# Performance work log

Measured on AMD Instinct MI355X. Metric: run time of the kernel, lower is better.

The kernel has to match this reference:

```python
import jax, jax.numpy as jnp
import numpy as np
from jax import lax

D_MODEL = 1024
D_STATE = 16
D_CONV = 4
EXPAND = 2
D_INNER = EXPAND * D_MODEL
LN_EPS = 1e-5


def setup_inputs() -> dict:
    key = jax.random.key(0)
    ks = jax.random.split(key, 12)
    B, L = 4, 1024
    s = lambda fan_in: 1.0 / np.sqrt(fan_in)
    inp = {
        "x": jax.random.normal(ks[0], (B, L, D_MODEL), jnp.float32),
        # in_proj: d_model -> 2*d_inner (stored as (in, out))
        "W_in": jax.random.normal(ks[1], (D_MODEL, 2 * D_INNER), jnp.float32) * s(D_MODEL),
        "b_in": jnp.zeros((2 * D_INNER,), jnp.float32),
        # depthwise causal conv1d, kernel (d_inner, 1, d_conv)
        "conv_w": jax.random.normal(ks[2], (D_INNER, 1, D_CONV), jnp.float32) * s(D_CONV),
        "conv_b": jnp.zeros((D_INNER,), jnp.float32),
        # x_proj: d_inner -> 2*d_state
        "W_xp": jax.random.normal(ks[3], (D_INNER, 2 * D_STATE), jnp.float32) * s(D_INNER),
        "b_xp": jnp.zeros((2 * D_STATE,), jnp.float32),
        # dt_proj: d_inner -> d_inner
        "W_dt": jax.random.normal(ks[4], (D_INNER, D_INNER), jnp.float32) * s(D_INNER),
        "b_dt": jnp.zeros((D_INNER,), jnp.float32),
        # A_log = log(arange(1, d_state+1)) repeated over d_inner
        "A_log": jnp.log(jnp.broadcast_to(jnp.arange(1, D_STATE + 1, dtype=jnp.float32), (D_INNER, D_STATE))),
        "D_param": jnp.ones((D_INNER,), jnp.float32),
        # out_proj: d_inner -> d_model
        "W_out": jax.random.normal(ks[5], (D_INNER, D_MODEL), jnp.float32) * s(D_INNER),
        "b_out": jnp.zeros((D_MODEL,), jnp.float32),
        "ln_g": jnp.ones((D_MODEL,), jnp.float32),
        "ln_b": jnp.zeros((D_MODEL,), jnp.float32),
    }
    return inp


def _causal_depthwise_conv(x, w, b):
    # x: (B, d_inner, L); w: (d_inner, 1, d_conv). Left-pad d_conv-1 => causal.
    y = lax.conv_general_dilated(
        x, w, window_strides=(1,), padding=[(D_CONV - 1, 0)],
        dimension_numbers=("NCH", "OIH", "NCH"), feature_group_count=D_INNER)
    return y + b[None, :, None]


def _ssm(x, A, Bm, Cm, dt, D_param):
    # x, dt: (B,L,D)  A: (D,N)  Bm, Cm: (B,L,N)
    A_disc = jnp.exp(dt[..., None] * A)               # (B,L,D,N)
    dBx = (dt * x)[..., None] * Bm[:, :, None, :]     # (B,L,D,N) = dt*B*x_t
    h0 = jnp.zeros(x.shape[:1] + A.shape, x.dtype)    # (B,D,N)

    def step(h, inputs):
        a, bx, c = inputs                              # (B,D,N),(B,D,N),(B,N)
        h = a * h + bx
        y = jnp.einsum("bdn,bn->bd", h, c)
        return h, y

    _, ys = lax.scan(step, h0, (jnp.swapaxes(A_disc, 0, 1),
                                jnp.swapaxes(dBx, 0, 1),
                                jnp.swapaxes(Cm, 0, 1)))
    y = jnp.swapaxes(ys, 0, 1)                         # (B,L,D)
    return y + x * D_param


def reference(x, W_in, b_in, conv_w, conv_b, W_xp, b_xp, W_dt, b_dt,
              A_log, D_param, W_out, b_out, ln_g, ln_b):
    residual = x
    xr = x @ W_in + b_in                               # (B,L,2*d_inner)
    xi, res = jnp.split(xr, 2, axis=-1)
    xi = jax.nn.silu(xi)
    xi = jnp.swapaxes(xi, 1, 2)                        # (B,d_inner,L)
    xi = _causal_depthwise_conv(xi, conv_w, conv_b)
    xi = jnp.swapaxes(xi, 1, 2)
    xi = jax.nn.silu(xi)
    bc = xi @ W_xp + b_xp                              # (B,L,2*d_state)
    Bm, Cm = jnp.split(bc, 2, axis=-1)
    dt = jax.nn.softplus(xi @ W_dt + b_dt)
    A = -jnp.exp(A_log)                                # (d_inner, d_state)
    y = _ssm(xi, A, Bm, Cm, dt, D_param)
    y = y * jax.nn.silu(res)
    out = y @ W_out + b_out
    z = out + residual
    mu = jnp.mean(z, axis=-1, keepdims=True)
    var = jnp.var(z, axis=-1, keepdims=True)
    return (z - mu) * jax.lax.rsqrt(var + LN_EPS) * ln_g + ln_b
```

## Files before the change

### kernel.cpp

```cpp
#include <hip/hip_runtime.h>
#include <math.h>

#define D_MODEL 1024
#define D_INNER 2048
#define D_STATE 16
#define D_CONV  4
#define NCHUNK  16
#define LCHUNK  64

typedef unsigned short u16;
typedef __attribute__((ext_vector_type(8))) short short8;
typedef __attribute__((ext_vector_type(4))) float f32x4;
typedef __attribute__((ext_vector_type(4))) unsigned short u16x4;

__device__ __forceinline__ float silu_f(float x) { return x / (1.f + __expf(-x)); }
__device__ __forceinline__ float softplus_f(float x) {
    return fmaxf(x, 0.f) + log1pf(__expf(-fabsf(x)));
}
__device__ __forceinline__ u16 f2bf(float f) {
    union { float f; unsigned u; } c; c.f = f;
    unsigned r = c.u + 0x7fffu + ((c.u >> 16) & 1u);
    return (u16)(r >> 16);
}
__device__ __forceinline__ float bf2f(u16 v) {
    union { unsigned u; float f; } c; c.u = ((unsigned)v) << 16; return c.f;
}
__device__ __forceinline__ void gload_lds16(const void* g, void* l) {
    __builtin_amdgcn_global_load_lds((const __attribute__((address_space(1))) void*)g,
                                     (__attribute__((address_space(3))) void*)l, 16, 0, 0);
}

__global__ __launch_bounds__(256)
void f32_to_bf16_kernel(const float* __restrict__ in, u16* __restrict__ out, int n4)
{
    const int i = blockIdx.x * 256 + threadIdx.x;
    if (i >= n4) return;
    const float4 v = *(const float4*)&in[(size_t)i * 4];
    u16x4 o; o.x = f2bf(v.x); o.y = f2bf(v.y); o.z = f2bf(v.z); o.w = f2bf(v.w);
    *(u16x4*)&out[(size_t)i * 4] = o;
}

__global__ __launch_bounds__(256)
void transpose_bf16_kernel(const float* __restrict__ W, u16* __restrict__ Wt, int K, int N)
{
    __shared__ float tile[32][33];
    const int tx = threadIdx.x & 31, ty = threadIdx.x >> 5;
    const int n0 = blockIdx.x * 32, k0 = blockIdx.y * 32;
#pragma unroll
    for (int q = 0; q < 4; q++)
        tile[ty + q * 8][tx] = W[(size_t)(k0 + ty + q * 8) * N + n0 + tx];
    __syncthreads();
#pragma unroll
    for (int q = 0; q < 4; q++)
        Wt[(size_t)(n0 + ty + q * 8) * K + k0 + tx] = f2bf(tile[tx][ty + q * 8]);
}

template <int MODE>
__global__ __launch_bounds__(512, 2)
void gemm_mfma256(const u16* __restrict__ A, const u16* __restrict__ Bt,
                  const float* __restrict__ bias,
                  void* __restrict__ out0v, void* __restrict__ out1v,
                  int M, int N, int K)
{
    __shared__ __align__(16) short As[2][256 * 64];
    __shared__ __align__(16) short Bs[2][256 * 64];

    const int tid = threadIdx.x;
    const int wid = tid >> 6, lane = tid & 63;
    const int wr = wid >> 2, wc = wid & 3;
    const int row0 = blockIdx.y * 256, col0 = blockIdx.x * 256;
    const int kg = lane >> 4, r16 = lane & 15;

    f32x4 acc[8][4] = {};

    const u16* Abase = A + (size_t)row0 * K;
    const u16* Bbase = Bt + (size_t)col0 * K;

#define STAGE256(bi, kk) do {                                                   \
        _Pragma("unroll")                                                       \
        for (int q = 0; q < 4; q++) {                                           \
            const int c = (q << 9) + tid;                                       \
            const int r = c >> 3;                                               \
            const int ks8 = (((c & 7) ^ (r & 7)) << 3);                         \
            gload_lds16(Abase + (size_t)r * K + (kk) + ks8,                     \
                        &As[bi][(((q << 9) + (wid << 6))) << 3]);               \
            gload_lds16(Bbase + (size_t)r * K + (kk) + ks8,                     \
                        &Bs[bi][(((q << 9) + (wid << 6))) << 3]);               \
        }                                                                       \
    } while (0)

    const int nt = K >> 6;
    STAGE256(0, 0);
    asm volatile("s_waitcnt vmcnt(0)" ::: "memory");
    __builtin_amdgcn_s_barrier();

    int cur = 0;
    for (int t = 0; t < nt; ++t) {
        if (t + 1 < nt) STAGE256(cur ^ 1, (t + 1) << 6);

        const int rx = r16 & 7;
#pragma unroll
        for (int ks = 0; ks < 2; ks++) {
            const int sl8 = (((ks << 2) + kg) ^ rx) << 3;
            short8 af[8], bg[4];
#pragma unroll
            for (int i = 0; i < 8; i++) {
                const int r = wr * 128 + i * 16 + r16;
                af[i] = *(const short8*)&As[cur][r * 64 + sl8];
            }
#pragma unroll
            for (int j = 0; j < 4; j++) {
                const int r = wc * 64 + j * 16 + r16;
                bg[j] = *(const short8*)&Bs[cur][r * 64 + sl8];
            }
            __builtin_amdgcn_s_setprio(1);
#pragma unroll
            for (int i = 0; i < 8; i++)
#pragma unroll
                for (int j = 0; j < 4; j++)
                    acc[i][j] = __builtin_amdgcn_mfma_f32_16x16x32_bf16(af[i], bg[j], acc[i][j], 0, 0, 0);
            __builtin_amdgcn_s_setprio(0);
        }

        asm volatile("s_waitcnt vmcnt(0)" ::: "memory");
        __builtin_amdgcn_s_barrier();
        cur ^= 1;
    }
#undef STAGE256

#pragma unroll
    for (int i = 0; i < 8; i++) {
#pragma unroll
        for (int j = 0; j < 4; j++) {
#pragma unroll
            for (int r = 0; r < 4; r++) {
                const int row = row0 + wr * 128 + i * 16 + kg * 4 + r;
                const int col = col0 + wc * 64 + j * 16 + r16;
                float v = acc[i][j][r] + bias[col];
                if (MODE == 0) {
                    u16* o0 = (u16*)out0v; u16* o1 = (u16*)out1v;
                    if (col < D_INNER) o0[(size_t)row * D_INNER + col] = f2bf(silu_f(v));
                    else               o1[(size_t)row * D_INNER + (col - D_INNER)] = f2bf(v);
                } else {
                    ((float*)out0v)[(size_t)row * N + col] = softplus_f(v);
                }
            }
        }
    }
}

__global__ __launch_bounds__(256)
void gemm_mfma_128(const u16* __restrict__ A, const u16* __restrict__ Bt,
                   const float* __restrict__ bias, const float* __restrict__ aux,
                   float* __restrict__ out0, int M, int N, int K)
{
    __shared__ __align__(16) short As[3][4096];
    __shared__ __align__(16) short Bs[3][4096];

    const int tid = threadIdx.x;
    const int wid = tid >> 6, lane = tid & 63;
    const int wr = wid >> 1, wc = wid & 1;
    const int row0 = blockIdx.y * 128, col0 = blockIdx.x * 128;

    f32x4 acc[4][4] = {};

    const int c0 = wid * 128 + lane;
    const int c1 = c0 + 64;
    const u16* Abase = A + (size_t)row0 * K;
    const u16* Bbase = Bt + (size_t)col0 * K;

    const int gsl8 = (((lane & 3) ^ ((lane >> 3) & 3)) << 3);
    const int kg = lane >> 4, r16 = lane & 15;
    const int sl8 = ((kg ^ ((r16 >> 1) & 3)) << 3);

#define STAGE(bi, kk) do {                                                                   \
        gload_lds16(Abase + (size_t)(c0 >> 2) * K + (kk) + gsl8, &As[bi][wid * 1024]);       \
        gload_lds16(Abase + (size_t)(c1 >> 2) * K + (kk) + gsl8, &As[bi][wid * 1024 + 512]); \
        gload_lds16(Bbase + (size_t)(c0 >> 2) * K + (kk) + gsl8, &Bs[bi][wid * 1024]);       \
        gload_lds16(Bbase + (size_t)(c1 >> 2) * K + (kk) + gsl8, &Bs[bi][wid * 1024 + 512]); \
    } while (0)

    const int nt = K >> 5;
    STAGE(0, 0);
    STAGE(1, 32);
    int cs = 0;
    for (int t = 0; t < nt; ++t) {
        if (t + 2 < nt) {
            const int ss = (cs + 2 >= 3) ? cs - 1 : cs + 2;
            STAGE(ss, (t + 2) << 5);
            asm volatile("s_waitcnt vmcnt(8)" ::: "memory");
        } else if (t + 1 < nt) {
            asm volatile("s_waitcnt vmcnt(4)" ::: "memory");
        } else {
            asm volatile("s_waitcnt vmcnt(0)" ::: "memory");
        }
        __builtin_amdgcn_s_barrier();

        short8 af[4], bg[4];
#pragma unroll
        for (int i = 0; i < 4; i++) {
            const int r = wr * 64 + i * 16 + r16;
            af[i] = *(const short8*)&As[cs][r * 32 + sl8];
        }
#pragma unroll
        for (int j = 0; j < 4; j++) {
            const int r = wc * 64 + j * 16 + r16;
            bg[j] = *(const short8*)&Bs[cs][r * 32 + sl8];
        }
        __builtin_amdgcn_s_setprio(1);
#pragma unroll
        for (int i = 0; i < 4; i++)
#pragma unroll
            for (int j = 0; j < 4; j++)
                acc[i][j] = __builtin_amdgcn_mfma_f32_16x16x32_bf16(af[i], bg[j], acc[i][j], 0, 0, 0);
        __builtin_amdgcn_s_setprio(0);

        asm volatile("s_waitcnt lgkmcnt(0)" ::: "memory");
        __builtin_amdgcn_s_barrier();
        cs = (cs + 1 >= 3) ? 0 : cs + 1;
    }
#undef STAGE

#pragma unroll
    for (int i = 0; i < 4; i++) {
#pragma unroll
        for (int j = 0; j < 4; j++) {
#pragma unroll
            for (int r = 0; r < 4; r++) {
                const int row = row0 + wr * 64 + i * 16 + kg * 4 + r;
                const int col = col0 + wc * 64 + j * 16 + r16;
                float v = acc[i][j][r] + bias[col];
                out0[(size_t)row * N + col] = v + aux[(size_t)row * N + col];
            }
        }
    }
}

__global__ __launch_bounds__(256)
void conv_silu_kernel(const u16* __restrict__ xi, const float* __restrict__ w,
                      const float* __restrict__ cb, float* __restrict__ xc,
                      u16* __restrict__ xcb, int total)
{
    const int i = blockIdx.x * 256 + threadIdx.x;
    if (i >= total) return;
    const int d = i & (D_INNER - 1);
    const int l = (i >> 11) & 1023;
    float acc = cb[d];
#pragma unroll
    for (int k = 0; k < D_CONV; k++) {
        const int li = l + k - (D_CONV - 1);
        if (li >= 0) acc = fmaf(w[d * D_CONV + k], bf2f(xi[(size_t)i + (k - (D_CONV - 1)) * D_INNER]), acc);
    }
    const float s = silu_f(acc);
    xc[i] = s;
    xcb[i] = f2bf(s);
}

__global__ __launch_bounds__(256)
void xproj_mfma_kernel(const u16* __restrict__ A, const u16* __restrict__ Wt,
                       const float* __restrict__ bxp, float* __restrict__ bc)
{
    const int wid = threadIdx.x >> 6, lane = threadIdx.x & 63;
    const int kg = lane >> 4, r16 = lane & 15;
    const int tok0 = blockIdx.x * 64 + wid * 16;

    f32x4 acc[2] = {};
#pragma unroll 4
    for (int k0 = 0; k0 < D_INNER; k0 += 32) {
        const short8 a  = *(const short8*)&A[(size_t)(tok0 + r16) * D_INNER + k0 + kg * 8];
        const short8 b0 = *(const short8*)&Wt[(size_t)r16 * D_INNER + k0 + kg * 8];
        const short8 b1 = *(const short8*)&Wt[(size_t)(16 + r16) * D_INNER + k0 + kg * 8];
        acc[0] = __builtin_amdgcn_mfma_f32_16x16x32_bf16(a, b0, acc[0], 0, 0, 0);
        acc[1] = __builtin_amdgcn_mfma_f32_16x16x32_bf16(a, b1, acc[1], 0, 0, 0);
    }
#pragma unroll
    for (int j = 0; j < 2; j++)
#pragma unroll
        for (int r = 0; r < 4; r++) {
            const int token = tok0 + kg * 4 + r;
            const int c = j * 16 + r16;
            bc[(size_t)token * 32 + c] = acc[j][r] + bxp[c];
        }
}

__global__ __launch_bounds__(256)
void ssm_s1_kernel(const float* __restrict__ xc, const float* __restrict__ dt,
                   const float* __restrict__ bc, const float* __restrict__ A_log,
                   float* __restrict__ hend, float* __restrict__ dtsum)
{
    const int tid = threadIdx.x;
    const int ch = tid >> 4, n = tid & 15;
    const int d0 = blockIdx.x * 16;
    const int c = blockIdx.y;
    const int b = blockIdx.z;
    const int d = d0 + ch;

    const float Aln = -__expf(A_log[d * D_STATE + n]);

    __shared__ float sdt[64][16], sdtx[64][16], sB[64][16];

    float h = 0.f, S = 0.f;

    const int l0 = c * LCHUNK;
    {
        const int l = tid >> 2, di = (tid & 3) << 2;
        const size_t g = ((size_t)(b * 1024 + l0 + l)) * D_INNER + d0 + di;
        const float4 dv = *(const float4*)&dt[g];
        const float4 xv = *(const float4*)&xc[g];
        float4 dx;
        dx.x = dv.x * xv.x; dx.y = dv.y * xv.y; dx.z = dv.z * xv.z; dx.w = dv.w * xv.w;
        *(float4*)&sdt[l][di] = dv;
        *(float4*)&sdtx[l][di] = dx;
        *(float4*)&sB[l][di] = *(const float4*)&bc[((size_t)(b * 1024 + l0 + l)) * 32 + di];
    }
    __syncthreads();
#pragma unroll 16
    for (int l = 0; l < 64; l++) {
        const float dtv = sdt[l][ch];
        const float a = __expf(dtv * Aln);
        h = fmaf(a, h, sdtx[l][ch] * sB[l][n]);
        S += dtv;
    }
    hend[((size_t)(b * NCHUNK + c) * D_INNER + d) * D_STATE + n] = h;
    if (n == 0) dtsum[(size_t)(b * NCHUNK + c) * D_INNER + d] = S;
}

__global__ __launch_bounds__(256)
void ssm_s3_kernel(const float* __restrict__ xc, const float* __restrict__ dt,
                   const float* __restrict__ bc, const float* __restrict__ A_log,
                   const float* __restrict__ Dp, const u16* __restrict__ resbf,
                   const float* __restrict__ hend, const float* __restrict__ dtsum,
                   u16* __restrict__ ybf)
{
    const int tid = threadIdx.x;
    const int wid = tid >> 6, lane = tid & 63;
    const int ch4 = lane >> 4, n = lane & 15;
    const int ch = wid * 4 + ch4;
    const int d0 = blockIdx.x * 16;
    const int c = blockIdx.y;
    const int b = blockIdx.z;
    const int d = d0 + ch;

    const float Aln = -__expf(A_log[d * D_STATE + n]);
    const float Dv = Dp[d];

    float h = 0.f;
    for (int cc = 0; cc < c; cc++) {
        const float S = dtsum[(size_t)(b * NCHUNK + cc) * D_INNER + d];
        const float P = __expf(Aln * S);
        h = fmaf(P, h, hend[((size_t)(b * NCHUNK + cc) * D_INNER + d) * D_STATE + n]);
    }

    __shared__ float sdt[64][16], sdtx[64][16], sx[64][16], sres[64][16];
    __shared__ float sbc[64][32];
    __shared__ float pbuf[4 * 16 * 68];

    float* pw = &pbuf[wid * 16 * 68];

    const int l0 = c * LCHUNK;
    {
        const int l = tid >> 2, di = (tid & 3) << 2;
        const size_t g = ((size_t)(b * 1024 + l0 + l)) * D_INNER + d0 + di;
        const float4 dv = *(const float4*)&dt[g];
        const float4 xv = *(const float4*)&xc[g];
        const u16x4 rv = *(const u16x4*)&resbf[g];
        float4 dx;
        dx.x = dv.x * xv.x; dx.y = dv.y * xv.y; dx.z = dv.z * xv.z; dx.w = dv.w * xv.w;
        *(float4*)&sdt[l][di] = dv;
        *(float4*)&sdtx[l][di] = dx;
        *(float4*)&sx[l][di] = xv;
        sres[l][di + 0] = bf2f(rv.x);
        sres[l][di + 1] = bf2f(rv.y);
        sres[l][di + 2] = bf2f(rv.z);
        sres[l][di + 3] = bf2f(rv.w);
        const int r0 = tid >> 3, c4 = (tid & 7) << 2;
        *(float4*)&sbc[r0][c4] = *(const float4*)&bc[((size_t)(b * 1024 + l0 + r0)) * 32 + c4];
        const int r1 = (tid + 256) >> 3;
        *(float4*)&sbc[r1][c4] = *(const float4*)&bc[((size_t)(b * 1024 + l0 + r1)) * 32 + c4];
    }
    __syncthreads();

    for (int l16 = 0; l16 < 4; l16++) {
#pragma unroll
        for (int j = 0; j < 16; j++) {
            const int l = l16 * 16 + j;
            const float dtv = sdt[l][ch];
            const float a = __expf(dtv * Aln);
            h = fmaf(a, h, sdtx[l][ch] * sbc[l][n]);
            pw[j * 68 + ch4 * 16 + n] = h * sbc[l][16 + n];
        }
        __builtin_amdgcn_wave_barrier();
        const float4 q0 = *(const float4*)&pw[n * 68 + ch4 * 16 + 0];
        const float4 q1 = *(const float4*)&pw[n * 68 + ch4 * 16 + 4];
        const float4 q2 = *(const float4*)&pw[n * 68 + ch4 * 16 + 8];
        const float4 q3 = *(const float4*)&pw[n * 68 + ch4 * 16 + 12];
        const float sum = ((q0.x + q0.y) + (q0.z + q0.w)) + ((q1.x + q1.y) + (q1.z + q1.w))
                        + ((q2.x + q2.y) + (q2.z + q2.w)) + ((q3.x + q3.y) + (q3.z + q3.w));
        const int t = l16 * 16 + n;
        const float xv = sx[t][ch];
        const float rv = sres[t][ch];
        const float yv = (sum + xv * Dv) * silu_f(rv);
        ybf[((size_t)(b * 1024 + l0 + t)) * D_INNER + d] = f2bf(yv);
        __builtin_amdgcn_wave_barrier();
    }
}

__global__ __launch_bounds__(256)
void layernorm_kernel(const float* __restrict__ z, const float* __restrict__ g,
                      const float* __restrict__ beta, float* __restrict__ out)
{
    const int row = blockIdx.x;
    const int tid = threadIdx.x;
    const float* zr = z + (size_t)row * D_MODEL;
    const float4 v = *(const float4*)&zr[tid << 2];
    float s = v.x + v.y + v.z + v.w;
    float ss = v.x * v.x + v.y * v.y + v.z * v.z + v.w * v.w;

    __shared__ float sm[256], sq[256];
    sm[tid] = s; sq[tid] = ss;
    __syncthreads();
    for (int off = 128; off > 0; off >>= 1) {
        if (tid < off) { sm[tid] += sm[tid + off]; sq[tid] += sq[tid + off]; }
        __syncthreads();
    }
    const float mean = sm[0] * (1.f / D_MODEL);
    const float var = sq[0] * (1.f / D_MODEL) - mean * mean;
    const float rstd = rsqrtf(var + 1e-5f);

    float4 o;
    o.x = (v.x - mean) * rstd * g[(tid << 2) + 0] + beta[(tid << 2) + 0];
    o.y = (v.y - mean) * rstd * g[(tid << 2) + 1] + beta[(tid << 2) + 1];
    o.z = (v.z - mean) * rstd * g[(tid << 2) + 2] + beta[(tid << 2) + 2];
    o.w = (v.w - mean) * rstd * g[(tid << 2) + 3] + beta[(tid << 2) + 3];
    *(float4*)&out[(size_t)row * D_MODEL + (tid << 2)] = o;
}

extern "C" void kernel_launch(void* const* d_in, const int* in_sizes, int n_in,
                              void* d_out, int out_size, void* d_ws, size_t ws_size,
                              hipStream_t stream)
{
    const float* x      = (const float*)d_in[0];
    const float* W_in   = (const float*)d_in[1];
    const float* b_in   = (const float*)d_in[2];
    const float* conv_w = (const float*)d_in[3];
    const float* conv_b = (const float*)d_in[4];
    const float* W_xp   = (const float*)d_in[5];
    const float* b_xp   = (const float*)d_in[6];
    const float* W_dt   = (const float*)d_in[7];
    const float* b_dt   = (const float*)d_in[8];
    const float* A_log  = (const float*)d_in[9];
    const float* D_par  = (const float*)d_in[10];
    const float* W_out  = (const float*)d_in[11];
    const float* b_out  = (const float*)d_in[12];
    const float* ln_g   = (const float*)d_in[13];
    const float* ln_b   = (const float*)d_in[14];
    float* out = (float*)d_out;

    const int BL = in_sizes[0] / D_MODEL;
    const int Bb = BL / 1024;
    const size_t BLD = (size_t)BL * D_INNER;

    float* ws    = (float*)d_ws;
    float* xcb   = ws;
    float* dtb   = xcb + BLD;
    float* bcbuf = dtb + BLD;
    float* hend  = bcbuf + (size_t)BL * 32;
    float* dtsum = hend + (size_t)Bb * NCHUNK * D_INNER * D_STATE;
    u16*   xibf  = (u16*)(dtsum + (size_t)Bb * NCHUNK * D_INNER);
    u16*   resbf = xibf + BLD;
    u16*   xcbf  = resbf + BLD;
    u16*   xbf   = xcbf + BLD;
    u16*   wxpT  = xbf + (size_t)BL * D_MODEL;
    u16*   wtmp  = wxpT + 32 * D_INNER;
    u16*   ybf   = xibf;
    float* zbuf  = dtb;

    f32_to_bf16_kernel<<<(BL * D_MODEL / 4 + 255) / 256, 256, 0, stream>>>(x, xbf, BL * D_MODEL / 4);

    transpose_bf16_kernel<<<dim3(2 * D_INNER / 32, D_MODEL / 32), 256, 0, stream>>>(W_in, wtmp, D_MODEL, 2 * D_INNER);

    gemm_mfma256<0><<<dim3(2 * D_INNER / 256, BL / 256), 512, 0, stream>>>(
        xbf, wtmp, b_in, xibf, resbf, BL, 2 * D_INNER, D_MODEL);

    transpose_bf16_kernel<<<dim3(1, D_INNER / 32), 256, 0, stream>>>(W_xp, wxpT, D_INNER, 32);

    conv_silu_kernel<<<(int)(BLD / 256), 256, 0, stream>>>(
        xibf, conv_w, conv_b, xcb, xcbf, (int)BLD);

    xproj_mfma_kernel<<<BL / 64, 256, 0, stream>>>(xcbf, wxpT, b_xp, bcbuf);

    transpose_bf16_kernel<<<dim3(D_INNER / 32, D_INNER / 32), 256, 0, stream>>>(W_dt, wtmp, D_INNER, D_INNER);

    gemm_mfma256<1><<<dim3(D_INNER / 256, BL / 256), 512, 0, stream>>>(
        xcbf, wtmp, b_dt, dtb, nullptr, BL, D_INNER, D_INNER);

    ssm_s1_kernel<<<dim3(D_INNER / 16, NCHUNK, Bb), 256, 0, stream>>>(
        xcb, dtb, bcbuf, A_log, hend, dtsum);

    ssm_s3_kernel<<<dim3(D_INNER / 16, NCHUNK, Bb), 256, 0, stream>>>(
        xcb, dtb, bcbuf, A_log, D_par, resbf, hend, dtsum, ybf);

    transpose_bf16_kernel<<<dim3(D_MODEL / 32, D_INNER / 32), 256, 0, stream>>>(W_out, wtmp, D_INNER, D_MODEL);

    gemm_mfma_128<<<dim3(D_MODEL / 128, BL / 128), 256, 0, stream>>>(
        ybf, wtmp, b_out, x, zbuf, BL, D_MODEL, D_INNER);

    layernorm_kernel<<<BL, 256, 0, stream>>>(zbuf, ln_g, ln_b, out);
}
```

Measured before the change: 396.8 us.

## Split A/B staging in 256 GEMM and route dt_proj through 128-tile GEMM

Splits the 256-tile GEMM's prefetch into separate A and B stages: B for the next tile is issued after the first k-substep, and a partial vmcnt wait lets compute start before every load finishes. The aim is more overlap of global-to-LDS loads with MFMA work in the in_proj GEMM. Separately, the dt_proj GEMM (M=4096, N=K=2048) moves to the 128x128 tile kernel, now templated with a softplus epilogue. That gives 512 blocks instead of 128 for better CU occupancy, at the cost of less data reuse per block.

```diff
diff --git a/kernel.cpp b/kernel.cpp
--- a/kernel.cpp
+++ b/kernel.cpp
@@ -76,29 +76,42 @@
     const u16* Abase = A + (size_t)row0 * K;
     const u16* Bbase = Bt + (size_t)col0 * K;
 
-#define STAGE256(bi, kk) do {                                                   \
+#define STAGE_A(bi, kk) do {                                                    \
         _Pragma("unroll")                                                       \
         for (int q = 0; q < 4; q++) {                                           \
             const int c = (q << 9) + tid;                                       \
             const int r = c >> 3;                                               \
             const int ks8 = (((c & 7) ^ (r & 7)) << 3);                         \
             gload_lds16(Abase + (size_t)r * K + (kk) + ks8,                     \
-                        &As[bi][(((q << 9) + (wid << 6))) << 3]);               \
-            gload_lds16(Bbase + (size_t)r * K + (kk) + ks8,                     \
-                        &Bs[bi][(((q << 9) + (wid << 6))) << 3]);               \
+                        &As[bi][((q << 9) + (wid << 6)) << 3]);                 \
         }                                                                       \
     } while (0)
+#define STAGE_B(bi, kk) do {                                                    \
+        _Pragma("unroll")                                                       \
+        for (int q = 0; q < 4; q++) {                                           \
+            const int c = (q << 9) + tid;                                       \
+            const int r = c >> 3;                                               \
+            const int ks8 = (((c & 7) ^ (r & 7)) << 3);                         \
+            gload_lds16(Bbase + (size_t)r * K + (kk) + ks8,                     \
+                        &Bs[bi][((q << 9) + (wid << 6)) << 3]);                 \
+        }                                                                       \
+    } while (0)
 
     const int nt = K >> 6;
-    STAGE256(0, 0);
-    asm volatile("s_waitcnt vmcnt(0)" ::: "memory");
-    __builtin_amdgcn_s_barrier();
+    STAGE_A(0, 0);
+    STAGE_B(0, 0);
 
     int cur = 0;
+    const int rx = r16 & 7;
     for (int t = 0; t < nt; ++t) {
-        if (t + 1 < nt) STAGE256(cur ^ 1, (t + 1) << 6);
-
-        const int rx = r16 & 7;
+        if (t + 1 < nt) {
+            STAGE_A(cur ^ 1, (t + 1) << 6);
+            asm volatile("s_waitcnt vmcnt(4)" ::: "memory");
+        } else {
+            asm volatile("s_waitcnt vmcnt(0)" ::: "memory");
+        }
+        __builtin_amdgcn_s_barrier();
+
 #pragma unroll
         for (int ks = 0; ks < 2; ks++) {
             const int sl8 = (((ks << 2) + kg) ^ rx) << 3;
@@ -120,13 +133,16 @@
                 for (int j = 0; j < 4; j++)
                     acc[i][j] = __builtin_amdgcn_mfma_f32_16x16x32_bf16(af[i], bg[j], acc[i][j], 0, 0, 0);
             __builtin_amdgcn_s_setprio(0);
-        }
-
-        asm volatile("s_waitcnt vmcnt(0)" ::: "memory");
+            if (ks == 0 && t + 1 < nt)
+                STAGE_B(cur ^ 1, (t + 1) << 6);
+        }
+
+        asm volatile("s_waitcnt lgkmcnt(0)" ::: "memory");
         __builtin_amdgcn_s_barrier();
         cur ^= 1;
     }
-#undef STAGE256
+#undef STAGE_A
+#undef STAGE_B
 
 #pragma unroll
     for (int i = 0; i < 8; i++) {
@@ -149,6 +165,7 @@
     }
 }
 
+template <int MODE>
 __global__ __launch_bounds__(256)
 void gemm_mfma_128(const u16* __restrict__ A, const u16* __restrict__ Bt,
                    const float* __restrict__ bias, const float* __restrict__ aux,
@@ -230,7 +247,8 @@
                 const int row = row0 + wr * 64 + i * 16 + kg * 4 + r;
                 const int col = col0 + wc * 64 + j * 16 + r16;
                 float v = acc[i][j][r] + bias[col];
-                out0[(size_t)row * N + col] = v + aux[(size_t)row * N + col];
+                if (MODE == 1) out0[(size_t)row * N + col] = softplus_f(v);
+                else           out0[(size_t)row * N + col] = v + aux[(size_t)row * N + col];
             }
         }
     }
@@ -491,8 +509,8 @@
 
     transpose_bf16_kernel<<<dim3(D_INNER / 32, D_INNER / 32), 256, 0, stream>>>(W_dt, wtmp, D_INNER, D_INNER);
 
-    gemm_mfma256<1><<<dim3(D_INNER / 256, BL / 256), 512, 0, stream>>>(
-        xcbf, wtmp, b_dt, dtb, nullptr, BL, D_INNER, D_INNER);
+    gemm_mfma_128<1><<<dim3(D_INNER / 128, BL / 128), 256, 0, stream>>>(
+        xcbf, wtmp, b_dt, nullptr, dtb, BL, D_INNER, D_INNER);
 
     ssm_s1_kernel<<<dim3(D_INNER / 16, NCHUNK, Bb), 256, 0, stream>>>(
         xcb, dtb, bcbuf, A_log, hend, dtsum);
@@ -502,7 +520,7 @@
 
     transpose_bf16_kernel<<<dim3(D_MODEL / 32, D_INNER / 32), 256, 0, stream>>>(W_out, wtmp, D_INNER, D_MODEL);
 
-    gemm_mfma_128<<<dim3(D_MODEL / 128, BL / 128), 256, 0, stream>>>(
+    gemm_mfma_128<2><<<dim3(D_MODEL / 128, BL / 128), 256, 0, stream>>>(
         ybf, wtmp, b_out, x, zbuf, BL, D_MODEL, D_INNER);
 
     layernorm_kernel<<<BL, 256, 0, stream>>>(zbuf, ln_g, ln_b, out);
```

Result: faster. 359.1 us (-9.5%).
